# Performance work log

Hardware: AMD Instinct MI355X
Metric: run time of the kernel (lower is better)

## Reference

```python
import jax, jax.numpy as jnp
import numpy as np

KMAX = 16


def setup_inputs() -> dict:
    key = jax.random.key(0)
    k1, k2, k3 = jax.random.split(key, 3)
    B, S, D = 8, 2048, 128
    first_point = jax.random.normal(k1, (B, S, 3), dtype=jnp.float32)
    first_index = jnp.sort(
        jax.random.randint(k2, (B, S, 1), 0, 20000, dtype=jnp.int64), axis=1
    )
    attribute = jax.random.normal(k3, (B, S, D), dtype=jnp.float32)
    return {"first_point": first_point, "first_index": first_index, "attribute": attribute}


def _pairwise_sqdist(p):
    # p: [B, S, 3] -> [B, S, S]; loop over the 3 coordinate dims like the
    # original to avoid a [B, S, S, 3] intermediate.
    d2 = (p[..., 0][:, :, None] - p[..., 0][:, None, :]) ** 2
    for n in range(1, 3):
        d2 = d2 + (p[..., n][:, :, None] - p[..., n][:, None, :]) ** 2
    return d2


def reference(first_point, first_index, attribute):
    B, S, _ = first_point.shape
    # squared pairwise distances (squared=True branch)
    d2 = _pairwise_sqdist(first_point)                      # [B, S, S]
    # K nearest neighbors via full argsort (faithful to torch.argsort[:, :, :K])
    neighbors = jnp.argsort(d2, axis=-1)[:, :, :KMAX]       # [B, S, K]

    b_idx = jnp.arange(B)[:, None, None]                    # [B, 1, 1]

    # gather attributes of neighbors: [B, S, K, D]
    attr_nb = attribute[b_idx, neighbors]

    # 'distance' coordinate: gathered squared distances -> [B, S, K, 1]
    distance_neighbors = jnp.take_along_axis(d2, neighbors, axis=-1)[..., None]

    # 'index_distance' coordinate: |first_index - neighbor_index| -> [B, S, K, 1]
    nei_index = first_index[b_idx, neighbors]               # [B, S, K, 1]
    index_distance = jnp.abs(
        (first_index[:, :, None, :] - nei_index).astype(jnp.float32)
    )

    return (distance_neighbors, index_distance, attr_nb)
```

## Files before the change

### kernel.cpp

```cpp
#include <hip/hip_runtime.h>

#define NB 8
#define NS 2048
#define ND 128
#define NK 16

template <int CTRL>
__device__ inline double dpp_f64(double v) {
    long long b = __double_as_longlong(v);
    int lo = (int)(unsigned int)b;
    int hi = (int)(b >> 32);
    lo = __builtin_amdgcn_update_dpp(0, lo, CTRL, 0xF, 0xF, true);
    hi = __builtin_amdgcn_update_dpp(0, hi, CTRL, 0xF, 0xF, true);
    return __longlong_as_double(((long long)hi << 32) | (unsigned int)lo);
}

__device__ inline double shfl_xor_f64(double v, int mask) {
    long long b = __double_as_longlong(v);
    int lo = __shfl_xor((int)(unsigned int)b, mask, 64);
    int hi = __shfl_xor((int)(b >> 32), mask, 64);
    return __longlong_as_double(((long long)hi << 32) | (unsigned int)lo);
}

__device__ inline double wave_min_f64(double v) {
    v = fmin(v, dpp_f64<0xB1>(v));
    v = fmin(v, dpp_f64<0x4E>(v));
    v = fmin(v, dpp_f64<0x141>(v));
    v = fmin(v, dpp_f64<0x140>(v));
    v = fmin(v, shfl_xor_f64(v, 16));
    v = fmin(v, shfl_xor_f64(v, 32));
    return v;
}

__global__ __launch_bounds__(256) void knn_kernel(
    const float* __restrict__ pts,
    const int*   __restrict__ fidx,
    const float* __restrict__ attr,
    float*       __restrict__ out)
{
    __shared__ double sorted[4][64][17];

    const int wv   = threadIdx.x >> 6;
    const int lane = threadIdx.x & 63;
    const int row  = blockIdx.x * 4 + wv;
    const int b = row >> 11;
    const int i = row & 2047;

    const float* pb = pts + (size_t)b * NS * 3;
    const float qx = pb[i * 3 + 0];
    const float qy = pb[i * 3 + 1];
    const float qz = pb[i * 3 + 2];

    double keys[33];
#pragma unroll
    for (int t = 0; t < 32; ++t) {
        const int j = t * 64 + lane;
        const float x = pb[j * 3 + 0];
        const float y = pb[j * 3 + 1];
        const float z = pb[j * 3 + 2];
        const float dx = __fsub_rn(qx, x);
        const float dy = __fsub_rn(qy, y);
        const float dz = __fsub_rn(qz, z);
        float d = __fmul_rn(dx, dx);
        d = __fadd_rn(d, __fmul_rn(dy, dy));
        d = __fadd_rn(d, __fmul_rn(dz, dz));
        const unsigned int db = __float_as_uint(d);
        const unsigned int hi = 0x3FF00000u | (db >> 12);
        const unsigned int lo = (db << 20) | ((unsigned int)j << 9);
        keys[t] = __longlong_as_double(((long long)hi << 32) | lo);
    }

#pragma unroll
    for (int p = 1; p < 32; p <<= 1) {
#pragma unroll
        for (int k = p; k >= 1; k >>= 1) {
#pragma unroll
            for (int j = k & (p - 1); j + k < 32; j += 2 * k) {
#pragma unroll
                for (int ii = 0; ii < k; ++ii) {
                    const int a = ii + j;
                    const int c = ii + j + k;
                    if (c < 32 && (a / (2 * p)) == (c / (2 * p))) {
                        const double ka = keys[a];
                        const double kc = keys[c];
                        keys[a] = fmin(ka, kc);
                        keys[c] = fmax(ka, kc);
                    }
                }
            }
        }
    }

    double* myList = &sorted[wv][lane][0];
#pragma unroll
    for (int t = 0; t <= NK; ++t) myList[t] = keys[t];

    double h = keys[0];
    int hp = 0;
    double myKey = 0.0;
#pragma unroll
    for (int k = 0; k < NK; ++k) {
        const double mn = wave_min_f64(h);
        if (lane == k) myKey = mn;
        if (h == mn) {
            ++hp;
            h = myList[hp];
        }
    }

    float* out0 = out;
    float* out1 = out + (size_t)NB * NS * NK;
    float* out2 = out + (size_t)2 * NB * NS * NK;
    const size_t rowBase = (size_t)row * NK;

    const long long kb = __double_as_longlong(myKey);
    const int myJ = (int)((kb >> 9) & 0x7FF);

    if (lane < NK) {
        const unsigned int db = (unsigned int)(kb >> 20);
        out0[rowBase + lane] = __uint_as_float(db);
        const int ii = fidx[(size_t)b * NS + i];
        const int jj = fidx[(size_t)b * NS + myJ];
        out1[rowBase + lane] = fabsf((float)(ii - jj));
    }

    const int half = lane >> 5;
    const int comp = lane & 31;
    const float* ab = attr + (size_t)b * NS * ND;
    float* o2row = out2 + rowBase * ND;
#pragma unroll
    for (int p = 0; p < 8; ++p) {
        const unsigned int j0 = (unsigned int)__shfl(myJ, 2 * p, 64);
        const unsigned int j1 = (unsigned int)__shfl(myJ, 2 * p + 1, 64);
        const unsigned int jj = half ? j1 : j0;
        const float4 v = *(const float4*)(ab + (size_t)jj * ND + comp * 4);
        const int k = 2 * p + half;
        *(float4*)(o2row + (size_t)k * ND + comp * 4) = v;
    }
}

extern "C" void kernel_launch(void* const* d_in, const int* in_sizes, int n_in,
                              void* d_out, int out_size, void* d_ws, size_t ws_size,
                              hipStream_t stream) {
    const float* pts  = (const float*)d_in[0];
    const int*   fidx = (const int*)d_in[1];
    const float* attr = (const float*)d_in[2];
    float* out = (float*)d_out;

    const int rows = NB * NS;
    const int blocks = rows / 4;
    knn_kernel<<<blocks, 256, 0, stream>>>(pts, fidx, attr, out);
}
```

Baseline: 49.62 us.

## Replace full 32-key sort with half-sorts plus bitonic merge and register-buffered wave merge

Measured after the change: 52.40 us. 1.06x slower.

```diff
diff --git a/kernel.cpp b/kernel.cpp
--- a/kernel.cpp
+++ b/kernel.cpp
@@ -4,6 +4,8 @@
 #define NS 2048
 #define ND 128
 #define NK 16
+
+typedef float f32x4 __attribute__((ext_vector_type(4)));
 
 template <int CTRL>
 __device__ inline double dpp_f64(double v) {
@@ -32,6 +34,30 @@
     return v;
 }
 
+template <int N>
+__device__ inline void batcher_sort(double* k) {
+#pragma unroll
+    for (int p = 1; p < N; p <<= 1) {
+#pragma unroll
+        for (int kk = p; kk >= 1; kk >>= 1) {
+#pragma unroll
+            for (int j = kk & (p - 1); j + kk < N; j += 2 * kk) {
+#pragma unroll
+                for (int ii = 0; ii < kk; ++ii) {
+                    const int a = ii + j;
+                    const int c = ii + j + kk;
+                    if (c < N && (a / (2 * p)) == (c / (2 * p))) {
+                        const double ka = k[a];
+                        const double kc = k[c];
+                        k[a] = fmin(ka, kc);
+                        k[c] = fmax(ka, kc);
+                    }
+                }
+            }
+        }
+    }
+}
+
 __global__ __launch_bounds__(256) void knn_kernel(
     const float* __restrict__ pts,
     const int*   __restrict__ fidx,
@@ -51,7 +77,7 @@
     const float qy = pb[i * 3 + 1];
     const float qz = pb[i * 3 + 2];
 
-    double keys[33];
+    double keys[32];
 #pragma unroll
     for (int t = 0; t < 32; ++t) {
         const int j = t * 64 + lane;
@@ -70,42 +96,45 @@
         keys[t] = __longlong_as_double(((long long)hi << 32) | lo);
     }
 
+    batcher_sort<16>(keys);
+    batcher_sort<16>(keys + 16);
+    double c[16];
 #pragma unroll
-    for (int p = 1; p < 32; p <<= 1) {
+    for (int t = 0; t < 16; ++t) c[t] = fmin(keys[t], keys[31 - t]);
 #pragma unroll
-        for (int k = p; k >= 1; k >>= 1) {
+    for (int d = 8; d >= 1; d >>= 1) {
 #pragma unroll
-            for (int j = k & (p - 1); j + k < 32; j += 2 * k) {
-#pragma unroll
-                for (int ii = 0; ii < k; ++ii) {
-                    const int a = ii + j;
-                    const int c = ii + j + k;
-                    if (c < 32 && (a / (2 * p)) == (c / (2 * p))) {
-                        const double ka = keys[a];
-                        const double kc = keys[c];
-                        keys[a] = fmin(ka, kc);
-                        keys[c] = fmax(ka, kc);
-                    }
-                }
+        for (int t = 0; t < 16; ++t) {
+            if ((t & d) == 0 && (t | d) < 16) {
+                const double ka = c[t];
+                const double kc = c[t | d];
+                c[t] = fmin(ka, kc);
+                c[t | d] = fmax(ka, kc);
             }
         }
     }
 
-    double* myList = &sorted[wv][lane][0];
+    const double PAD = __longlong_as_double(0x7FE0000000000000LL);
+    double* myLds = &sorted[wv][lane][0];
 #pragma unroll
-    for (int t = 0; t <= NK; ++t) myList[t] = keys[t];
+    for (int t = 0; t < 12; ++t) myLds[t] = c[t + 4];
+#pragma unroll
+    for (int t = 12; t < 16; ++t) myLds[t] = PAD;
 
-    double h = keys[0];
+    double w0 = c[0], w1 = c[1], w2 = c[2], w3 = c[3];
     int hp = 0;
     double myKey = 0.0;
 #pragma unroll
     for (int k = 0; k < NK; ++k) {
-        const double mn = wave_min_f64(h);
+        const double rd = myLds[hp];
+        const double mn = wave_min_f64(w0);
         if (lane == k) myKey = mn;
-        if (h == mn) {
-            ++hp;
-            h = myList[hp];
-        }
+        const bool pop = (w0 == mn);
+        w0 = pop ? w1 : w0;
+        w1 = pop ? w2 : w1;
+        w2 = pop ? w3 : w2;
+        w3 = pop ? rd : w3;
+        hp += pop ? 1 : 0;
     }
 
     float* out0 = out;
@@ -128,14 +157,20 @@
     const int comp = lane & 31;
     const float* ab = attr + (size_t)b * NS * ND;
     float* o2row = out2 + rowBase * ND;
+
+    unsigned int jj8[8];
+#pragma unroll
+    for (int p = 0; p < 8; ++p)
+        jj8[p] = (unsigned int)__shfl(myJ, 2 * p + half, 64);
+
+    f32x4 cur = *(const f32x4*)(ab + (size_t)jj8[0] * ND + comp * 4);
 #pragma unroll
     for (int p = 0; p < 8; ++p) {
-        const unsigned int j0 = (unsigned int)__shfl(myJ, 2 * p, 64);
-        const unsigned int j1 = (unsigned int)__shfl(myJ, 2 * p + 1, 64);
-        const unsigned int jj = half ? j1 : j0;
-        const float4 v = *(const float4*)(ab + (size_t)jj * ND + comp * 4);
-        const int k = 2 * p + half;
-        *(float4*)(o2row + (size_t)k * ND + comp * 4) = v;
+        f32x4 nxt = cur;
+        if (p < 7) nxt = *(const f32x4*)(ab + (size_t)jj8[p + 1] * ND + comp * 4);
+        __builtin_nontemporal_store(
+            cur, (f32x4*)(o2row + (size_t)(2 * p + half) * ND + comp * 4));
+        cur = nxt;
     }
 }
 
```
